# Optimization experiments

Measured on AMD Instinct MI355X. Metric: run time of the kernel, lower is better.

The kernel has to match this reference:

```python
import jax, jax.numpy as jnp
import numpy as np

BITS = 8
CLIP_BOUND = 2.0 ** (BITS - 1) - 1.0  # 127 for int8
EPS = 1e-12


def _per_tensor_scale(x):
    # Dynamic per-tensor abs-max calibration (TensorQuantizer.update with
    # calibration over the whole tensor): scale maps abs-max to the clip bound.
    amax = jnp.max(jnp.abs(x))
    return CLIP_BOUND / jnp.maximum(amax, EPS)


def setup_inputs() -> dict:
    key = jax.random.key(0)
    k1, k2 = jax.random.split(key)
    lhs = jax.random.normal(k1, (4096, 4096), dtype=jnp.float32)
    rhs = jax.random.normal(k2, (4096, 4096), dtype=jnp.float32)
    return {"lhs": lhs, "rhs": rhs}


def reference(lhs, rhs):
    # --- calibration (scales are statistics, no gradient flows through them) ---
    ls = _per_tensor_scale(lhs)
    rs = _per_tensor_scale(rhs)

    # --- quantize to int8 grid ---
    ql = jnp.clip(jnp.round(lhs * ls), -CLIP_BOUND, CLIP_BOUND).astype(jnp.int8)
    qr = jnp.clip(jnp.round(rhs * rs), -CLIP_BOUND, CLIP_BOUND).astype(jnp.int8)

    # --- integer dot_general with int32 accumulation (aqt_dot_general core) ---
    dimension_numbers = (((1,), (0,)), ((), ()))
    acc = jax.lax.dot_general(
        ql, qr, dimension_numbers, preferred_element_type=jnp.int32
    )

    # --- dequantize by product of scales ---
    out = acc.astype(jnp.float32) / (ls * rs)
    return out
```

## Files before the change

### kernel.cpp

```cpp
#include <hip/hip_runtime.h>
#include <stdint.h>


#define NROW 4096
#define NELEM (4096 * 4096)

typedef __attribute__((ext_vector_type(4))) int int32x4;
typedef __attribute__((ext_vector_type(16))) int int32x16;

__global__ void absmax_both_kernel(const float* __restrict__ lhs,
                                   const float* __restrict__ rhs,
                                   unsigned* __restrict__ amax) {
    __shared__ float red[4];
    const int t = blockIdx.x & 1;
    const float4* x4 = (const float4*)(t ? rhs : lhs);
    const int bid = blockIdx.x >> 1;
    const int stride = (gridDim.x >> 1) * blockDim.x;
    int i = bid * blockDim.x + threadIdx.x;
    float m0 = 0.0f, m1 = 0.0f, m2 = 0.0f, m3 = 0.0f;
    for (; i + 3 * stride < NELEM / 4; i += 4 * stride) {
        float4 a = x4[i];
        float4 b = x4[i + stride];
        float4 c = x4[i + 2 * stride];
        float4 d = x4[i + 3 * stride];
        m0 = fmaxf(m0, fmaxf(fmaxf(fabsf(a.x), fabsf(a.y)),
                             fmaxf(fabsf(a.z), fabsf(a.w))));
        m1 = fmaxf(m1, fmaxf(fmaxf(fabsf(b.x), fabsf(b.y)),
                             fmaxf(fabsf(b.z), fabsf(b.w))));
        m2 = fmaxf(m2, fmaxf(fmaxf(fabsf(c.x), fabsf(c.y)),
                             fmaxf(fabsf(c.z), fabsf(c.w))));
        m3 = fmaxf(m3, fmaxf(fmaxf(fabsf(d.x), fabsf(d.y)),
                             fmaxf(fabsf(d.z), fabsf(d.w))));
    }
    for (; i < NELEM / 4; i += stride) {
        float4 a = x4[i];
        m0 = fmaxf(m0, fmaxf(fmaxf(fabsf(a.x), fabsf(a.y)),
                             fmaxf(fabsf(a.z), fabsf(a.w))));
    }
    float m = fmaxf(fmaxf(m0, m1), fmaxf(m2, m3));
    for (int off = 32; off > 0; off >>= 1)
        m = fmaxf(m, __shfl_down(m, off, 64));
    const int lane = threadIdx.x & 63, wave = threadIdx.x >> 6;
    if (lane == 0) red[wave] = m;
    __syncthreads();
    if (threadIdx.x == 0) {
        float b = fmaxf(fmaxf(red[0], red[1]), fmaxf(red[2], red[3]));
        atomicMax(amax + t, __float_as_uint(b));
    }
}

__device__ __forceinline__ int q8(float v, float s) {
    int r = __float2int_rn(v * s);
    r = r < -127 ? -127 : r;
    r = r > 127 ? 127 : r;
    return r;
}

__device__ __forceinline__ int pack4(float a, float b, float c, float d,
                                     float s) {
    return (q8(a, s) & 0xff) | ((q8(b, s) & 0xff) << 8) |
           ((q8(c, s) & 0xff) << 16) | ((q8(d, s) & 0xff) << 24);
}

__global__ void quant_kernel(const float* __restrict__ lhs,
                             const float* __restrict__ rhs,
                             int8_t* __restrict__ qA, int8_t* __restrict__ qT,
                             const unsigned* __restrict__ amax) {
    __shared__ int8_t sm[64][68];
    if (blockIdx.x < 4096) {
        const float s = 127.0f / fmaxf(__uint_as_float(amax[0]), 1e-12f);
        const int c = blockIdx.x * 256 + threadIdx.x;
        const int l = c & 63;
        const int ks_g = (c >> 6) & 127;
        const int mt_g = c >> 13;
        const int row = mt_g * 32 + (l & 31);
        const int kb = ks_g * 32 + (l >> 5) * 16;
        const float4* src = (const float4*)(lhs + (size_t)row * NROW + kb);
        float4 v0 = src[0], v1 = src[1], v2 = src[2], v3 = src[3];
        int4 w;
        w.x = pack4(v0.x, v0.y, v0.z, v0.w, s);
        w.y = pack4(v1.x, v1.y, v1.z, v1.w, s);
        w.z = pack4(v2.x, v2.y, v2.z, v2.w, s);
        w.w = pack4(v3.x, v3.y, v3.z, v3.w, s);
        *(int4*)(qA + (size_t)c * 16) = w;
    } else {
        const float s = 127.0f / fmaxf(__uint_as_float(amax[1]), 1e-12f);
        const int b = blockIdx.x - 4096;
        const int n0 = (b & 63) * 64, k0 = (b >> 6) * 64;
        const int rl = threadIdx.x >> 4;
        const int nq = threadIdx.x & 15;
        for (int r = 0; r < 4; ++r) {
            const int kl = r * 16 + rl;
            float4 v = *(const float4*)(rhs + (size_t)(k0 + kl) * NROW + n0 + nq * 4);
            sm[nq * 4 + 0][kl] = (int8_t)q8(v.x, s);
            sm[nq * 4 + 1][kl] = (int8_t)q8(v.y, s);
            sm[nq * 4 + 2][kl] = (int8_t)q8(v.z, s);
            sm[nq * 4 + 3][kl] = (int8_t)q8(v.w, s);
        }
        __syncthreads();
        const int nt_l = threadIdx.x >> 7;
        const int ks_l = (threadIdx.x >> 6) & 1;
        const int l = threadIdx.x & 63;
        const int n_loc = nt_l * 32 + (l & 31);
        const int k_loc = ks_l * 32 + (l >> 5) * 16;
        int4 w;
        w.x = *(const int*)&sm[n_loc][k_loc + 0];
        w.y = *(const int*)&sm[n_loc][k_loc + 4];
        w.z = *(const int*)&sm[n_loc][k_loc + 8];
        w.w = *(const int*)&sm[n_loc][k_loc + 12];
        const int nt_g = (b & 63) * 2 + nt_l;
        const int ks_g = (b >> 6) * 2 + ks_l;
        *(int4*)(qT + (((size_t)nt_g * 128 + ks_g) * 64 + l) * 16) = w;
    }
}

__global__ __launch_bounds__(512, 2) void gemm_i8_kernel(
    const int8_t* __restrict__ qA, const int8_t* __restrict__ qBT,
    float* __restrict__ out, const unsigned* __restrict__ amax) {
    const int tid = threadIdx.x;
    const int lane = tid & 63;
    const int wave = tid >> 6;
    const int wm = wave >> 2;
    const int wn = wave & 3;

    const int bid = blockIdx.y * 16 + blockIdx.x;
    const int swz = (bid & 7) * 32 + (bid >> 3);
    const int m0 = (swz >> 4) * 256, n0 = (swz & 15) * 256;

    const int rl = lane & 31;
    const int hi = lane >> 5;

    const int8_t* pa = qA + ((size_t)(m0 / 32 + wm * 4) * 128 + 0) * 1024 + lane * 16;
    const int8_t* pb = qBT + ((size_t)(n0 / 32 + wn * 2) * 128 + 0) * 1024 + lane * 16;

    int32x16 acc[4][2];
#pragma unroll
    for (int mt = 0; mt < 4; ++mt)
#pragma unroll
        for (int nt = 0; nt < 2; ++nt) acc[mt][nt] = (int32x16)(0);

    int32x4 a0[4], b0[2], a1[4], b1[2];

#define LOADF(A, B, S)                                                        \
    {                                                                         \
        const int8_t* ap = pa + (S)*1024;                                     \
        const int8_t* bp = pb + (S)*1024;                                     \
        A[0] = *(const int32x4*)(ap);                                         \
        A[1] = *(const int32x4*)(ap + 131072);                                \
        A[2] = *(const int32x4*)(ap + 262144);                                \
        A[3] = *(const int32x4*)(ap + 393216);                                \
        B[0] = *(const int32x4*)(bp);                                         \
        B[1] = *(const int32x4*)(bp + 131072);                                \
    }

#define MFMAF(A, B)                                                           \
    {                                                                         \
        __builtin_amdgcn_s_setprio(1);                                        \
        _Pragma("unroll") for (int mt = 0; mt < 4; ++mt)                      \
            _Pragma("unroll") for (int nt = 0; nt < 2; ++nt) acc[mt][nt] =    \
                __builtin_amdgcn_mfma_i32_32x32x32_i8(A[mt], B[nt],           \
                                                      acc[mt][nt], 0, 0, 0);  \
        __builtin_amdgcn_s_setprio(0);                                        \
    }

    LOADF(a0, b0, 0)
#pragma unroll 1
    for (int s = 0; s < 126; s += 2) {
        LOADF(a1, b1, s + 1)
        MFMAF(a0, b0)
        LOADF(a0, b0, s + 2)
        MFMAF(a1, b1)
    }
    LOADF(a1, b1, 127)
    MFMAF(a0, b0)
    MFMAF(a1, b1)

    const float ls = 127.0f / fmaxf(__uint_as_float(amax[0]), 1e-12f);
    const float rs = 127.0f / fmaxf(__uint_as_float(amax[1]), 1e-12f);
    const float inv = 1.0f / (ls * rs);
#pragma unroll
    for (int mt = 0; mt < 4; ++mt)
#pragma unroll
        for (int nt = 0; nt < 2; ++nt)
#pragma unroll
            for (int reg = 0; reg < 16; ++reg) {
                const int row = m0 + wm * 128 + mt * 32 + (reg & 3) +
                                8 * (reg >> 2) + 4 * hi;
                const int col = n0 + wn * 64 + nt * 32 + rl;
                out[(size_t)row * NROW + col] = (float)acc[mt][nt][reg] * inv;
            }
#undef LOADF
#undef MFMAF
}

extern "C" void kernel_launch(void* const* d_in, const int* in_sizes, int n_in,
                              void* d_out, int out_size, void* d_ws,
                              size_t ws_size, hipStream_t stream) {
    const float* lhs = (const float*)d_in[0];
    const float* rhs = (const float*)d_in[1];
    float* out = (float*)d_out;

    int8_t* qA = (int8_t*)d_ws;
    int8_t* qBT = qA + (size_t)16 * 1024 * 1024;
    unsigned* amax = (unsigned*)(qBT + (size_t)16 * 1024 * 1024);

    hipMemsetAsync(amax, 0, 8, stream);
    absmax_both_kernel<<<2048, 256, 0, stream>>>(lhs, rhs, amax);
    quant_kernel<<<4096 + 4096, 256, 0, stream>>>(lhs, rhs, qA, qBT, amax);
    gemm_i8_kernel<<<dim3(16, 16), 512, 0, stream>>>(qA, qBT, out, amax);
}
```

Before: 142.4 us.

## Stage GEMM operand tiles through double-buffered LDS with direct global-to-LDS loads

The int8 GEMM no longer has every wave load its own MFMA fragments straight from global memory. Each block now cooperatively copies its A and B K-slab into shared memory with global_load_lds, double-buffered, and waves read fragments from LDS. This removes redundant global/L2 fetches of the same fragments by waves that share rows or columns. The cost is 128KB of LDS per block, which likely limits a CU to one block, plus a full block barrier and vmcnt drain on every K-step.

```diff
diff --git a/kernel.cpp b/kernel.cpp
--- a/kernel.cpp
+++ b/kernel.cpp
@@ -7,6 +7,8 @@
 
 typedef __attribute__((ext_vector_type(4))) int int32x4;
 typedef __attribute__((ext_vector_type(16))) int int32x16;
+typedef const __attribute__((address_space(1))) int8_t* gptr1_t;
+typedef __attribute__((address_space(3))) int8_t* lptr3_t;
 
 __global__ void absmax_both_kernel(const float* __restrict__ lhs,
                                    const float* __restrict__ rhs,
@@ -117,6 +119,9 @@
 __global__ __launch_bounds__(512, 2) void gemm_i8_kernel(
     const int8_t* __restrict__ qA, const int8_t* __restrict__ qBT,
     float* __restrict__ out, const unsigned* __restrict__ amax) {
+    __shared__ __align__(16) int8_t sA[2][32768];
+    __shared__ __align__(16) int8_t sB[2][32768];
+
     const int tid = threadIdx.x;
     const int lane = tid & 63;
     const int wave = tid >> 6;
@@ -130,8 +135,26 @@
     const int rl = lane & 31;
     const int hi = lane >> 5;
 
-    const int8_t* pa = qA + ((size_t)(m0 / 32 + wm * 4) * 128 + 0) * 1024 + lane * 16;
-    const int8_t* pb = qBT + ((size_t)(n0 / 32 + wn * 2) * 128 + 0) * 1024 + lane * 16;
+    const gptr1_t pA0 = (gptr1_t)(qA + (size_t)(m0 / 32 + (tid >> 8)) * 131072 +
+                                  (tid & 255) * 16);
+    const gptr1_t pB0 = (gptr1_t)(qBT + (size_t)(n0 / 32 + (tid >> 8)) * 131072 +
+                                  (tid & 255) * 16);
+    int8_t* sAf = &sA[0][0];
+    int8_t* sBf = &sB[0][0];
+    const int dst0 = tid * 16;
+
+    auto stage = [&](int slot, int kt) {
+        const int kb = kt * 4096;
+#pragma unroll
+        for (int j = 0; j < 4; ++j) {
+            __builtin_amdgcn_global_load_lds(
+                pA0 + (size_t)j * 262144 + kb,
+                (lptr3_t)(sAf + slot * 32768 + dst0 + j * 8192), 16, 0, 0);
+            __builtin_amdgcn_global_load_lds(
+                pB0 + (size_t)j * 262144 + kb,
+                (lptr3_t)(sBf + slot * 32768 + dst0 + j * 8192), 16, 0, 0);
+        }
+    };
 
     int32x16 acc[4][2];
 #pragma unroll
@@ -139,41 +162,46 @@
 #pragma unroll
         for (int nt = 0; nt < 2; ++nt) acc[mt][nt] = (int32x16)(0);
 
-    int32x4 a0[4], b0[2], a1[4], b1[2];
-
-#define LOADF(A, B, S)                                                        \
-    {                                                                         \
-        const int8_t* ap = pa + (S)*1024;                                     \
-        const int8_t* bp = pb + (S)*1024;                                     \
-        A[0] = *(const int32x4*)(ap);                                         \
-        A[1] = *(const int32x4*)(ap + 131072);                                \
-        A[2] = *(const int32x4*)(ap + 262144);                                \
-        A[3] = *(const int32x4*)(ap + 393216);                                \
-        B[0] = *(const int32x4*)(bp);                                         \
-        B[1] = *(const int32x4*)(bp + 131072);                                \
-    }
-
-#define MFMAF(A, B)                                                           \
-    {                                                                         \
-        __builtin_amdgcn_s_setprio(1);                                        \
-        _Pragma("unroll") for (int mt = 0; mt < 4; ++mt)                      \
-            _Pragma("unroll") for (int nt = 0; nt < 2; ++nt) acc[mt][nt] =    \
-                __builtin_amdgcn_mfma_i32_32x32x32_i8(A[mt], B[nt],           \
-                                                      acc[mt][nt], 0, 0, 0);  \
-        __builtin_amdgcn_s_setprio(0);                                        \
-    }
-
-    LOADF(a0, b0, 0)
+    const int aBase = wm * 16384 + lane * 16;
+    const int bBase = wn * 8192 + lane * 16;
+
+    auto compute = [&](const int8_t* a, const int8_t* b) {
+#pragma unroll
+        for (int ks = 0; ks < 4; ++ks) {
+            int32x4 af[4], bf[2];
+#pragma unroll
+            for (int mt = 0; mt < 4; ++mt)
+                af[mt] = *(const int32x4*)(a + aBase + mt * 4096 + ks * 1024);
+#pragma unroll
+            for (int nt = 0; nt < 2; ++nt)
+                bf[nt] = *(const int32x4*)(b + bBase + nt * 4096 + ks * 1024);
+            __builtin_amdgcn_s_setprio(1);
+#pragma unroll
+            for (int mt = 0; mt < 4; ++mt)
+#pragma unroll
+                for (int nt = 0; nt < 2; ++nt)
+                    acc[mt][nt] = __builtin_amdgcn_mfma_i32_32x32x32_i8(
+                        af[mt], bf[nt], acc[mt][nt], 0, 0, 0);
+            __builtin_amdgcn_s_setprio(0);
+        }
+    };
+
+    stage(0, 0);
+    asm volatile("s_waitcnt vmcnt(0)" ::: "memory");
+    __builtin_amdgcn_sched_barrier(0);
+    __builtin_amdgcn_s_barrier();
+    __builtin_amdgcn_sched_barrier(0);
+
 #pragma unroll 1
-    for (int s = 0; s < 126; s += 2) {
-        LOADF(a1, b1, s + 1)
-        MFMAF(a0, b0)
-        LOADF(a0, b0, s + 2)
-        MFMAF(a1, b1)
-    }
-    LOADF(a1, b1, 127)
-    MFMAF(a0, b0)
-    MFMAF(a1, b1)
+    for (int w = 0; w < 31; ++w) {
+        stage((w + 1) & 1, w + 1);
+        compute(sAf + (w & 1) * 32768, sBf + (w & 1) * 32768);
+        asm volatile("s_waitcnt vmcnt(0)" ::: "memory");
+        __builtin_amdgcn_sched_barrier(0);
+        __builtin_amdgcn_s_barrier();
+        __builtin_amdgcn_sched_barrier(0);
+    }
+    compute(sAf + 32768, sBf + 32768);
 
     const float ls = 127.0f / fmaxf(__uint_as_float(amax[0]), 1e-12f);
     const float rs = 127.0f / fmaxf(__uint_as_float(amax[1]), 1e-12f);
@@ -189,8 +217,6 @@
                 const int col = n0 + wn * 64 + nt * 32 + rl;
                 out[(size_t)row * NROW + col] = (float)acc[mt][nt][reg] * inv;
             }
-#undef LOADF
-#undef MFMAF
 }
 
 extern "C" void kernel_launch(void* const* d_in, const int* in_sizes, int n_in,
```

New measurement: 137.1 us. 1.04x faster.
